# Kernel optimization log

Hardware: AMD Instinct MI355X
Metric: run time of the kernel (lower is better)

Reference implementation:

```python
import jax, jax.numpy as jnp
import numpy as np

HIDDEN = 768
INNER = 512
EPS = 1e-5


def setup_inputs() -> dict:
    key = jax.random.key(0)
    ks = jax.random.split(key, 6)
    B, S = 8, 4096
    x = jax.random.normal(ks[0], (B, S, HIDDEN), dtype=jnp.float32)
    W1 = jax.random.normal(ks[1], (INNER, HIDDEN), dtype=jnp.float32) * 0.02
    b1 = jnp.zeros((INNER,), dtype=jnp.float32)
    W2 = jax.random.normal(ks[2], (HIDDEN, INNER), dtype=jnp.float32) * 0.02
    b2 = jnp.zeros((HIDDEN,), dtype=jnp.float32)
    # output_proj: nn.Linear(hidden, hidden)
    bound = 1.0 / np.sqrt(HIDDEN)
    Wo = jax.random.uniform(ks[3], (HIDDEN, HIDDEN), minval=-bound, maxval=bound, dtype=jnp.float32)
    bo = jax.random.uniform(ks[4], (HIDDEN,), minval=-bound, maxval=bound, dtype=jnp.float32)
    # LayerNorm affine params
    gamma = jnp.ones((HIDDEN,), dtype=jnp.float32)
    beta = jnp.zeros((HIDDEN,), dtype=jnp.float32)
    return {"x": x, "W1": W1, "b1": b1, "W2": W2, "b2": b2,
            "Wo": Wo, "bo": bo, "gamma": gamma, "beta": beta}


def reference(x, W1, b1, W2, b2, Wo, bo, gamma, beta):
    # NOTE: the torch module's inner 'TTT update' loop never actually modifies
    # W1/b1/W2/b2 (loss computed, no step applied), so the math per token is
    # independent and fully vectorizable across (batch, seq).
    h = jax.nn.relu(jnp.einsum('bsd,id->bsi', x, W1) + b1)       # [B,S,INNER]
    pred = jnp.einsum('bsi,di->bsd', h, W2) + b2                 # [B,S,HIDDEN]
    out = jnp.einsum('bsd,ed->bse', pred, Wo) + bo               # output_proj
    # LayerNorm over last dim
    mu = jnp.mean(out, axis=-1, keepdims=True)
    var = jnp.mean(jnp.square(out - mu), axis=-1, keepdims=True)
    out = (out - mu) * jax.lax.rsqrt(var + EPS) * gamma + beta
    return out
```

## Files before the change

### kernel.cpp

```cpp
#include <hip/hip_runtime.h>
#include <hip/hip_bf16.h>


#define HIDDEN 768
#define INNER  512

typedef __bf16 bf16_t;
typedef bf16_t bf16x8 __attribute__((ext_vector_type(8)));
typedef bf16_t bf16x4 __attribute__((ext_vector_type(4)));
typedef float  f32x4  __attribute__((ext_vector_type(4)));

__device__ __forceinline__ void async16(const void* g, void* lds) {
  __builtin_amdgcn_global_load_lds(
      (const __attribute__((address_space(1))) unsigned int*)g,
      (__attribute__((address_space(3))) unsigned int*)lds, 16, 0, 0);
}

__global__ __launch_bounds__(256)
void prep(const float* __restrict__ x, const float* __restrict__ W1,
          const float* __restrict__ W2, const float* __restrict__ Wo,
          const float* __restrict__ b2, const float* __restrict__ bo,
          bf16_t* __restrict__ xb, bf16_t* __restrict__ W1b,
          bf16_t* __restrict__ W2t, bf16_t* __restrict__ Wob,
          float* __restrict__ beq, int xb_blocks) {
  __shared__ float T[64][65];
  const int b = blockIdx.x, t = threadIdx.x;

  const float4* src; bf16x4* dst; int base;
  if (b < xb_blocks)           { src = (const float4*)x;  dst = (bf16x4*)xb;  base = b * 4096; }
  else if (b < xb_blocks + 24) { src = (const float4*)W1; dst = (bf16x4*)W1b; base = (b - xb_blocks) * 4096; }
  else if (b < xb_blocks + 60) { src = (const float4*)Wo; dst = (bf16x4*)Wob; base = (b - xb_blocks - 24) * 4096; }
  else if (b < xb_blocks + 156) {
    const int tile = b - xb_blocks - 60;
    const int d0 = (tile >> 3) << 6;
    const int i0 = (tile & 7) << 6;
#pragma unroll
    for (int j = 0; j < 4; ++j) {
      const int idx = j * 256 + t;
      const int r = idx >> 4, c4 = idx & 15;
      float4 v = *(const float4*)(W2 + (size_t)(d0 + r) * INNER + i0 + c4 * 4);
      T[r][c4 * 4 + 0] = v.x; T[r][c4 * 4 + 1] = v.y;
      T[r][c4 * 4 + 2] = v.z; T[r][c4 * 4 + 3] = v.w;
    }
    __syncthreads();
    const int i = t & 63, h4 = t >> 6;
    bf16x8 o0, o1;
#pragma unroll
    for (int c = 0; c < 8; ++c) { o0[c] = (bf16_t)T[h4 * 16 + c][i]; o1[c] = (bf16_t)T[h4 * 16 + 8 + c][i]; }
    bf16_t* orow = W2t + (size_t)(i0 + i) * HIDDEN + d0 + h4 * 16;
    *(bf16x8*)orow = o0;
    *(bf16x8*)(orow + 8) = o1;
    return;
  } else {
    const int e = (b - xb_blocks - 156) * 4 + (t >> 6);
    const int l = t & 63;
    float s = 0.f;
#pragma unroll
    for (int j = 0; j < 12; ++j) s += Wo[(size_t)e * HIDDEN + j * 64 + l] * b2[j * 64 + l];
#pragma unroll
    for (int off = 1; off < 64; off <<= 1) s += __shfl_xor(s, off, 64);
    if (l == 0) beq[e] = s + bo[e];
    return;
  }
#pragma unroll
  for (int i = 0; i < 16; ++i) {
    float4 v = src[base + i * 256 + t];
    bf16x4 o;
    o[0] = (bf16_t)v.x; o[1] = (bf16_t)v.y; o[2] = (bf16_t)v.z; o[3] = (bf16_t)v.w;
    dst[base + i * 256 + t] = o;
  }
}

__global__ __launch_bounds__(256, 2)
void gemm_weq(const bf16_t* __restrict__ A, const bf16_t* __restrict__ Bt,
              bf16_t* __restrict__ Cout) {
  constexpr int N_ = INNER, K_ = HIDDEN, NT = N_ / 128, T = K_ / 64;
  __shared__ __align__(16) bf16_t As[2][128 * 64];
  __shared__ __align__(16) bf16_t Bs[2][128 * 64];

  const int nb = blockIdx.x;
  const int m0 = (nb / NT) * 128;
  const int n0 = (nb % NT) * 128;

  const int tid = threadIdx.x;
  const int w = tid >> 6, l = tid & 63;
  const int wr = w >> 1, wc = w & 1;
  const int fr = l & 15, fq = l >> 4;

#define STAGEW(dst, src, r0, k0)                                              \
  _Pragma("unroll") for (int i = 0; i < 4; ++i) {                             \
    const int G = i * 256 + tid, row = G >> 3, g = G & 7;                     \
    async16((src) + (size_t)((r0) + row) * K_ + (k0) + ((g ^ (row & 7)) << 3),\
            (char*)(dst) + (size_t)(i * 256 + w * 64) * 16);                  \
  }

  STAGEW(As[0], A, m0, 0); STAGEW(Bs[0], Bt, n0, 0);
  __syncthreads();

  f32x4 acc[4][4] = {};
#pragma unroll
  for (int t = 0; t < T; ++t) {
    const int cur = t & 1;
    if (t < T - 1) {
      STAGEW(As[cur ^ 1], A, m0, (t + 1) * 64);
      STAGEW(Bs[cur ^ 1], Bt, n0, (t + 1) * 64);
    }
#pragma unroll
    for (int kk = 0; kk < 2; ++kk) {
      bf16x8 ax[4], bx[4];
#pragma unroll
      for (int m = 0; m < 4; ++m) {
        const int row = wr * 64 + m * 16 + fr;
        const int slot = (kk * 4 + fq) ^ (row & 7);
        ax[m] = *(const bf16x8*)((const char*)As[cur] + row * 128 + slot * 16);
      }
#pragma unroll
      for (int n = 0; n < 4; ++n) {
        const int row = wc * 64 + n * 16 + fr;
        const int slot = (kk * 4 + fq) ^ (row & 7);
        bx[n] = *(const bf16x8*)((const char*)Bs[cur] + row * 128 + slot * 16);
      }
#pragma unroll
      for (int m = 0; m < 4; ++m)
#pragma unroll
        for (int n = 0; n < 4; ++n)
          acc[m][n] = __builtin_amdgcn_mfma_f32_16x16x32_bf16(ax[m], bx[n], acc[m][n], 0, 0, 0);
    }
    __syncthreads();
  }
#undef STAGEW

  const int orow0 = m0 + wr * 64 + fq * 4;
  const int ocol0 = n0 + wc * 64 + fr;
#pragma unroll
  for (int n = 0; n < 4; ++n)
#pragma unroll
    for (int m = 0; m < 4; ++m)
#pragma unroll
      for (int j = 0; j < 4; ++j)
        Cout[(size_t)(orow0 + m * 16 + j) * N_ + ocol0 + n * 16] = (bf16_t)acc[m][n][j];
}

template <int N_, int K_, int MODE>
__global__ __launch_bounds__(256, 2)
void gemm_bt(const bf16_t* __restrict__ A, const bf16_t* __restrict__ Bt,
             const float* __restrict__ bias, bf16_t* __restrict__ Cout) {
  constexpr int NT = N_ / 128;
  constexpr int T  = K_ / 64;
  __shared__ __align__(16) bf16_t As[2][128 * 64];
  __shared__ __align__(16) bf16_t Bs[2][128 * 64];

  const int per = gridDim.x >> 3;
  const int nb  = (blockIdx.x & 7) * per + (blockIdx.x >> 3);
  const int m0 = (nb / NT) * 128;
  const int n0 = (nb % NT) * 128;

  const int tid = threadIdx.x;
  const int w = tid >> 6, l = tid & 63;
  const int wr = w >> 1, wc = w & 1;
  const int fr = l & 15, fq = l >> 4;

#define STAGE(dst, src, r0, k0)                                               \
  _Pragma("unroll") for (int i = 0; i < 4; ++i) {                             \
    const int G = i * 256 + tid, row = G >> 3, g = G & 7;                     \
    async16((src) + (size_t)((r0) + row) * K_ + (k0) + ((g ^ (row & 7)) << 3),\
            (char*)(dst) + (size_t)(i * 256 + w * 64) * 16);                  \
  }

  STAGE(As[0], A, m0, 0); STAGE(Bs[0], Bt, n0, 0);

  f32x4 acc[4][4] = {};
#pragma unroll
  for (int t = 0; t < T; ++t) {
    const int cur = t & 1;
    if (t + 1 < T) {
      STAGE(As[cur ^ 1], A, m0, (t + 1) * 64);
      STAGE(Bs[cur ^ 1], Bt, n0, (t + 1) * 64);
      asm volatile("s_waitcnt vmcnt(8)" ::: "memory");
    } else {
      asm volatile("s_waitcnt vmcnt(0)" ::: "memory");
    }
    __builtin_amdgcn_s_barrier();
#pragma unroll
    for (int kk = 0; kk < 2; ++kk) {
      bf16x8 ax[4], bx[4];
#pragma unroll
      for (int m = 0; m < 4; ++m) {
        const int row = wr * 64 + m * 16 + fr;
        const int slot = (kk * 4 + fq) ^ (row & 7);
        ax[m] = *(const bf16x8*)((const char*)As[cur] + row * 128 + slot * 16);
      }
#pragma unroll
      for (int n = 0; n < 4; ++n) {
        const int row = wc * 64 + n * 16 + fr;
        const int slot = (kk * 4 + fq) ^ (row & 7);
        bx[n] = *(const bf16x8*)((const char*)Bs[cur] + row * 128 + slot * 16);
      }
#pragma unroll
      for (int m = 0; m < 4; ++m)
#pragma unroll
        for (int n = 0; n < 4; ++n)
          acc[m][n] = __builtin_amdgcn_mfma_f32_16x16x32_bf16(ax[m], bx[n], acc[m][n], 0, 0, 0);
    }
    __builtin_amdgcn_s_barrier();
  }
#undef STAGE

  const int orow0 = m0 + wr * 64 + fq * 4;
  const int ocol0 = n0 + wc * 64 + fr;
#pragma unroll
  for (int n = 0; n < 4; ++n) {
    const int col = ocol0 + n * 16;
    const float bv = bias[col];
#pragma unroll
    for (int m = 0; m < 4; ++m)
#pragma unroll
      for (int j = 0; j < 4; ++j) {
        float v = acc[m][n][j] + bv;
        if (MODE == 0) v = fmaxf(v, 0.f);
        Cout[(size_t)(orow0 + m * 16 + j) * N_ + col] = (bf16_t)v;
      }
  }
}

__global__ __launch_bounds__(256)
void ln_bf16(const bf16_t* __restrict__ raw, const float* __restrict__ gamma,
             const float* __restrict__ beta, float* __restrict__ out) {
  const int r = blockIdx.x * 4 + (threadIdx.x >> 6);
  const int l = threadIdx.x & 63;
  const bf16_t* rp = raw + (size_t)r * HIDDEN;
  float v[12];
  float s = 0.f, q = 0.f;
#pragma unroll
  for (int c = 0; c < 3; ++c) {
    bf16x4 b4 = *(const bf16x4*)(rp + c * 256 + l * 4);
#pragma unroll
    for (int j = 0; j < 4; ++j) {
      const float f = (float)b4[j];
      v[c * 4 + j] = f; s += f; q += f * f;
    }
  }
#pragma unroll
  for (int off = 1; off < 64; off <<= 1) {
    s += __shfl_xor(s, off, 64);
    q += __shfl_xor(q, off, 64);
  }
  const float mu  = s * (1.0f / HIDDEN);
  const float var = fmaxf(q * (1.0f / HIDDEN) - mu * mu, 0.f);
  const float inv = rsqrtf(var + 1e-5f);
  float* op = out + (size_t)r * HIDDEN;
#pragma unroll
  for (int c = 0; c < 3; ++c) {
    float4 g = ((const float4*)gamma)[c * 64 + l];
    float4 b = ((const float4*)beta)[c * 64 + l];
    float4 o;
    o.x = (v[c * 4 + 0] - mu) * inv * g.x + b.x;
    o.y = (v[c * 4 + 1] - mu) * inv * g.y + b.y;
    o.z = (v[c * 4 + 2] - mu) * inv * g.z + b.z;
    o.w = (v[c * 4 + 3] - mu) * inv * g.w + b.w;
    ((float4*)op)[c * 64 + l] = o;
  }
}

extern "C" void kernel_launch(void* const* d_in, const int* in_sizes, int n_in,
                              void* d_out, int out_size, void* d_ws, size_t ws_size,
                              hipStream_t stream) {
  const float* x     = (const float*)d_in[0];
  const float* W1    = (const float*)d_in[1];
  const float* b1    = (const float*)d_in[2];
  const float* W2    = (const float*)d_in[3];
  const float* b2    = (const float*)d_in[4];
  const float* Wo    = (const float*)d_in[5];
  const float* bo    = (const float*)d_in[6];
  const float* gamma = (const float*)d_in[7];
  const float* beta  = (const float*)d_in[8];

  const int M = in_sizes[0] / HIDDEN;

  char* ws = (char*)d_ws;
  bf16_t* xb   = (bf16_t*)ws;
  bf16_t* raw  = xb;
  bf16_t* h    = (bf16_t*)(ws + (size_t)M * HIDDEN * 2);
  bf16_t* W1b  = (bf16_t*)(ws + (size_t)M * HIDDEN * 2 + (size_t)M * INNER * 2);
  bf16_t* W2t  = W1b + INNER * HIDDEN;
  bf16_t* Wob  = W2t + INNER * HIDDEN;
  bf16_t* Weq  = Wob + HIDDEN * HIDDEN;
  float*  beq  = (float*)(Weq + HIDDEN * INNER);

  const int xb_blocks = (M * HIDDEN / 4) / 4096;

  prep<<<xb_blocks + 156 + 192, 256, 0, stream>>>(x, W1, W2, Wo, b2, bo,
                                                  xb, W1b, W2t, Wob, beq, xb_blocks);
  gemm_weq<<<(HIDDEN / 128) * (INNER / 128), 256, 0, stream>>>(Wob, W2t, Weq);
  gemm_bt<INNER, HIDDEN, 0><<<(M / 128) * (INNER / 128), 256, 0, stream>>>(xb, W1b, b1, h);
  gemm_bt<HIDDEN, INNER, 1><<<(M / 128) * (HIDDEN / 128), 256, 0, stream>>>(h, Weq, beq, raw);
  ln_bf16<<<M / 4, 256, 0, stream>>>(raw, gamma, beta, (float*)d_out);
}
```

Measured before the change: 133.0 us.

## Enlarge GEMM tiles to 256x256 with 512-thread blocks and raise MFMA priority

Replaces the 128x128, 256-thread GEMM kernel with a 256x256 tile kernel using 8 waves, each computing 128x64 of output. Larger tiles raise arithmetic intensity and cut redundant global and L2 reads of A and B. The LDS read order is restructured so B fragments are loaded once and A fragments are streamed per row block, and s_setprio is raised around the MFMA section. The cost is 128KB of LDS per block and more accumulator registers, which leaves one block per CU and fewer blocks overall (256 or 384 for M=32768).

```diff
diff --git a/kernel.cpp b/kernel.cpp
--- a/kernel.cpp
+++ b/kernel.cpp
@@ -142,78 +142,82 @@
 }
 
 template <int N_, int K_, int MODE>
-__global__ __launch_bounds__(256, 2)
-void gemm_bt(const bf16_t* __restrict__ A, const bf16_t* __restrict__ Bt,
+__global__ __launch_bounds__(512, 1)
+void gemm256(const bf16_t* __restrict__ A, const bf16_t* __restrict__ Bt,
              const float* __restrict__ bias, bf16_t* __restrict__ Cout) {
-  constexpr int NT = N_ / 128;
+  constexpr int NT = N_ / 256;
   constexpr int T  = K_ / 64;
-  __shared__ __align__(16) bf16_t As[2][128 * 64];
-  __shared__ __align__(16) bf16_t Bs[2][128 * 64];
+  __shared__ __align__(16) bf16_t As[2][256 * 64];
+  __shared__ __align__(16) bf16_t Bs[2][256 * 64];
 
   const int per = gridDim.x >> 3;
   const int nb  = (blockIdx.x & 7) * per + (blockIdx.x >> 3);
-  const int m0 = (nb / NT) * 128;
-  const int n0 = (nb % NT) * 128;
+  const int m0 = (nb / NT) * 256;
+  const int n0 = (nb % NT) * 256;
 
   const int tid = threadIdx.x;
   const int w = tid >> 6, l = tid & 63;
-  const int wr = w >> 1, wc = w & 1;
+  const int wm = w >> 2, wn = w & 3;
   const int fr = l & 15, fq = l >> 4;
 
-#define STAGE(dst, src, r0, k0)                                               \
+#define STG(dst, src, r0, k0)                                                 \
   _Pragma("unroll") for (int i = 0; i < 4; ++i) {                             \
-    const int G = i * 256 + tid, row = G >> 3, g = G & 7;                     \
+    const int G = i * 512 + tid, row = G >> 3, g = G & 7;                     \
     async16((src) + (size_t)((r0) + row) * K_ + (k0) + ((g ^ (row & 7)) << 3),\
-            (char*)(dst) + (size_t)(i * 256 + w * 64) * 16);                  \
-  }
-
-  STAGE(As[0], A, m0, 0); STAGE(Bs[0], Bt, n0, 0);
-
-  f32x4 acc[4][4] = {};
+            (char*)(dst) + (size_t)(i * 512 + w * 64) * 16);                  \
+  }
+
+  STG(As[0], A, m0, 0); STG(Bs[0], Bt, n0, 0);
+
+  f32x4 acc[8][4] = {};
 #pragma unroll
   for (int t = 0; t < T; ++t) {
     const int cur = t & 1;
     if (t + 1 < T) {
-      STAGE(As[cur ^ 1], A, m0, (t + 1) * 64);
-      STAGE(Bs[cur ^ 1], Bt, n0, (t + 1) * 64);
+      STG(As[cur ^ 1], A, m0, (t + 1) * 64);
+      STG(Bs[cur ^ 1], Bt, n0, (t + 1) * 64);
       asm volatile("s_waitcnt vmcnt(8)" ::: "memory");
     } else {
       asm volatile("s_waitcnt vmcnt(0)" ::: "memory");
     }
     __builtin_amdgcn_s_barrier();
-#pragma unroll
-    for (int kk = 0; kk < 2; ++kk) {
-      bf16x8 ax[4], bx[4];
-#pragma unroll
-      for (int m = 0; m < 4; ++m) {
-        const int row = wr * 64 + m * 16 + fr;
+
+    __builtin_amdgcn_s_setprio(1);
+    bf16x8 bx[4][2];
+#pragma unroll
+    for (int n = 0; n < 4; ++n)
+#pragma unroll
+      for (int kk = 0; kk < 2; ++kk) {
+        const int row = wn * 64 + n * 16 + fr;
         const int slot = (kk * 4 + fq) ^ (row & 7);
-        ax[m] = *(const bf16x8*)((const char*)As[cur] + row * 128 + slot * 16);
-      }
+        bx[n][kk] = *(const bf16x8*)((const char*)Bs[cur] + row * 128 + slot * 16);
+      }
+#pragma unroll
+    for (int m = 0; m < 8; ++m) {
+      const int row = wm * 128 + m * 16 + fr;
+      const int s0 = fq ^ (row & 7);
+      const int s1 = (4 + fq) ^ (row & 7);
+      bf16x8 ax0 = *(const bf16x8*)((const char*)As[cur] + row * 128 + s0 * 16);
+      bf16x8 ax1 = *(const bf16x8*)((const char*)As[cur] + row * 128 + s1 * 16);
 #pragma unroll
       for (int n = 0; n < 4; ++n) {
-        const int row = wc * 64 + n * 16 + fr;
-        const int slot = (kk * 4 + fq) ^ (row & 7);
-        bx[n] = *(const bf16x8*)((const char*)Bs[cur] + row * 128 + slot * 16);
-      }
-#pragma unroll
-      for (int m = 0; m < 4; ++m)
-#pragma unroll
-        for (int n = 0; n < 4; ++n)
-          acc[m][n] = __builtin_amdgcn_mfma_f32_16x16x32_bf16(ax[m], bx[n], acc[m][n], 0, 0, 0);
-    }
+        acc[m][n] = __builtin_amdgcn_mfma_f32_16x16x32_bf16(ax0, bx[n][0], acc[m][n], 0, 0, 0);
+        acc[m][n] = __builtin_amdgcn_mfma_f32_16x16x32_bf16(ax1, bx[n][1], acc[m][n], 0, 0, 0);
+      }
+    }
+    __builtin_amdgcn_s_setprio(0);
     __builtin_amdgcn_s_barrier();
   }
-#undef STAGE
-
-  const int orow0 = m0 + wr * 64 + fq * 4;
-  const int ocol0 = n0 + wc * 64 + fr;
+#undef STG
+
+  const int orow0 = m0 + wm * 128 + fq * 4;
+  const int ocol0 = n0 + wn * 64 + fr;
 #pragma unroll
   for (int n = 0; n < 4; ++n) {
     const int col = ocol0 + n * 16;
     const float bv = bias[col];
 #pragma unroll
-    for (int m = 0; m < 4; ++m)
+    for (int m = 0; m < 8; ++m)
 #pragma unroll
       for (int j = 0; j < 4; ++j) {
         float v = acc[m][n][j] + bv;
@@ -292,7 +296,7 @@
   prep<<<xb_blocks + 156 + 192, 256, 0, stream>>>(x, W1, W2, Wo, b2, bo,
                                                   xb, W1b, W2t, Wob, beq, xb_blocks);
   gemm_weq<<<(HIDDEN / 128) * (INNER / 128), 256, 0, stream>>>(Wob, W2t, Weq);
-  gemm_bt<INNER, HIDDEN, 0><<<(M / 128) * (INNER / 128), 256, 0, stream>>>(xb, W1b, b1, h);
-  gemm_bt<HIDDEN, INNER, 1><<<(M / 128) * (HIDDEN / 128), 256, 0, stream>>>(h, Weq, beq, raw);
+  gemm256<INNER, HIDDEN, 0><<<(M / 256) * (INNER / 256), 512, 0, stream>>>(xb, W1b, b1, h);
+  gemm256<HIDDEN, INNER, 1><<<(M / 256) * (HIDDEN / 256), 512, 0, stream>>>(h, Weq, beq, raw);
   ln_bf16<<<M / 4, 256, 0, stream>>>(raw, gamma, beta, (float*)d_out);
 }
```

Measured after the change: 138.9 us. 4.5% more time.

## Fold Weq weight-product GEMM into prep kernel, dropping separate launch

Applied to the files above, without the earlier changes.

The product Wo·W2 is now computed directly inside the prep kernel by 24 blocks. These blocks read the fp32 weights straight from global memory, converting and transposing them on the fly, instead of first writing bf16 copies and then running a separate LDS-pipelined GEMM kernel. This removes one kernel launch and the intermediate Wob/W2t buffers. The cost is that the new blocks do uncached, strided scalar loads of W2 with no LDS staging, and they may become a long tail inside prep. The elementwise conversion path also batches all 16 loads before converting them, to expose more memory parallelism.

```diff
diff --git a/kernel.cpp b/kernel.cpp
--- a/kernel.cpp
+++ b/kernel.cpp
@@ -21,38 +21,57 @@
           const float* __restrict__ W2, const float* __restrict__ Wo,
           const float* __restrict__ b2, const float* __restrict__ bo,
           bf16_t* __restrict__ xb, bf16_t* __restrict__ W1b,
-          bf16_t* __restrict__ W2t, bf16_t* __restrict__ Wob,
-          float* __restrict__ beq, int xb_blocks) {
-  __shared__ float T[64][65];
+          bf16_t* __restrict__ Weq, float* __restrict__ beq, int xb_blocks) {
   const int b = blockIdx.x, t = threadIdx.x;
 
-  const float4* src; bf16x4* dst; int base;
-  if (b < xb_blocks)           { src = (const float4*)x;  dst = (bf16x4*)xb;  base = b * 4096; }
-  else if (b < xb_blocks + 24) { src = (const float4*)W1; dst = (bf16x4*)W1b; base = (b - xb_blocks) * 4096; }
-  else if (b < xb_blocks + 60) { src = (const float4*)Wo; dst = (bf16x4*)Wob; base = (b - xb_blocks - 24) * 4096; }
-  else if (b < xb_blocks + 156) {
-    const int tile = b - xb_blocks - 60;
-    const int d0 = (tile >> 3) << 6;
-    const int i0 = (tile & 7) << 6;
-#pragma unroll
-    for (int j = 0; j < 4; ++j) {
-      const int idx = j * 256 + t;
-      const int r = idx >> 4, c4 = idx & 15;
-      float4 v = *(const float4*)(W2 + (size_t)(d0 + r) * INNER + i0 + c4 * 4);
-      T[r][c4 * 4 + 0] = v.x; T[r][c4 * 4 + 1] = v.y;
-      T[r][c4 * 4 + 2] = v.z; T[r][c4 * 4 + 3] = v.w;
-    }
-    __syncthreads();
-    const int i = t & 63, h4 = t >> 6;
-    bf16x8 o0, o1;
-#pragma unroll
-    for (int c = 0; c < 8; ++c) { o0[c] = (bf16_t)T[h4 * 16 + c][i]; o1[c] = (bf16_t)T[h4 * 16 + 8 + c][i]; }
-    bf16_t* orow = W2t + (size_t)(i0 + i) * HIDDEN + d0 + h4 * 16;
-    *(bf16x8*)orow = o0;
-    *(bf16x8*)(orow + 8) = o1;
+  if (b < 24) {
+    const int m0 = (b >> 2) * 128;
+    const int n0 = (b & 3) * 128;
+    const int w = t >> 6, l = t & 63;
+    const int wr = w >> 1, wc = w & 1;
+    const int fr = l & 15, fq = l >> 4;
+
+    f32x4 acc[4][4] = {};
+    for (int k0 = 0; k0 < HIDDEN; k0 += 32) {
+      bf16x8 ax[4], bx[4];
+#pragma unroll
+      for (int m = 0; m < 4; ++m) {
+        const float* ap = Wo + (size_t)(m0 + wr * 64 + m * 16 + fr) * HIDDEN + k0 + fq * 8;
+        f32x4 p0 = *(const f32x4*)ap;
+        f32x4 p1 = *(const f32x4*)(ap + 4);
+        bf16x8 a;
+#pragma unroll
+        for (int c = 0; c < 4; ++c) { a[c] = (bf16_t)p0[c]; a[4 + c] = (bf16_t)p1[c]; }
+        ax[m] = a;
+      }
+#pragma unroll
+      for (int n = 0; n < 4; ++n) {
+        const float* bp = W2 + (size_t)(k0 + fq * 8) * INNER + n0 + wc * 64 + n * 16 + fr;
+        bf16x8 v;
+#pragma unroll
+        for (int c = 0; c < 8; ++c) v[c] = (bf16_t)bp[(size_t)c * INNER];
+        bx[n] = v;
+      }
+#pragma unroll
+      for (int m = 0; m < 4; ++m)
+#pragma unroll
+        for (int n = 0; n < 4; ++n)
+          acc[m][n] = __builtin_amdgcn_mfma_f32_16x16x32_bf16(ax[m], bx[n], acc[m][n], 0, 0, 0);
+    }
+    const int orow0 = m0 + wr * 64 + fq * 4;
+    const int ocol0 = n0 + wc * 64 + fr;
+#pragma unroll
+    for (int n = 0; n < 4; ++n)
+#pragma unroll
+      for (int m = 0; m < 4; ++m)
+#pragma unroll
+        for (int j = 0; j < 4; ++j)
+          Weq[(size_t)(orow0 + m * 16 + j) * INNER + ocol0 + n * 16] = (bf16_t)acc[m][n][j];
     return;
-  } else {
-    const int e = (b - xb_blocks - 156) * 4 + (t >> 6);
+  }
+
+  if (b >= 48 + xb_blocks) {
+    const int e = (b - 48 - xb_blocks) * 4 + (t >> 6);
     const int l = t & 63;
     float s = 0.f;
 #pragma unroll
@@ -62,83 +81,21 @@
     if (l == 0) beq[e] = s + bo[e];
     return;
   }
+
+  const float4* src; bf16x4* dst; int base;
+  if (b < 48) { src = (const float4*)W1; dst = (bf16x4*)W1b; base = (b - 24) * 4096; }
+  else        { src = (const float4*)x;  dst = (bf16x4*)xb;  base = (b - 48) * 4096; }
+
+  f32x4 v[16];
+#pragma unroll
+  for (int i = 0; i < 16; ++i) v[i] = *(const f32x4*)&src[base + i * 256 + t];
 #pragma unroll
   for (int i = 0; i < 16; ++i) {
-    float4 v = src[base + i * 256 + t];
     bf16x4 o;
-    o[0] = (bf16_t)v.x; o[1] = (bf16_t)v.y; o[2] = (bf16_t)v.z; o[3] = (bf16_t)v.w;
+    o[0] = (bf16_t)v[i][0]; o[1] = (bf16_t)v[i][1];
+    o[2] = (bf16_t)v[i][2]; o[3] = (bf16_t)v[i][3];
     dst[base + i * 256 + t] = o;
   }
-}
-
-__global__ __launch_bounds__(256, 2)
-void gemm_weq(const bf16_t* __restrict__ A, const bf16_t* __restrict__ Bt,
-              bf16_t* __restrict__ Cout) {
-  constexpr int N_ = INNER, K_ = HIDDEN, NT = N_ / 128, T = K_ / 64;
-  __shared__ __align__(16) bf16_t As[2][128 * 64];
-  __shared__ __align__(16) bf16_t Bs[2][128 * 64];
-
-  const int nb = blockIdx.x;
-  const int m0 = (nb / NT) * 128;
-  const int n0 = (nb % NT) * 128;
-
-  const int tid = threadIdx.x;
-  const int w = tid >> 6, l = tid & 63;
-  const int wr = w >> 1, wc = w & 1;
-  const int fr = l & 15, fq = l >> 4;
-
-#define STAGEW(dst, src, r0, k0)                                              \
-  _Pragma("unroll") for (int i = 0; i < 4; ++i) {                             \
-    const int G = i * 256 + tid, row = G >> 3, g = G & 7;                     \
-    async16((src) + (size_t)((r0) + row) * K_ + (k0) + ((g ^ (row & 7)) << 3),\
-            (char*)(dst) + (size_t)(i * 256 + w * 64) * 16);                  \
-  }
-
-  STAGEW(As[0], A, m0, 0); STAGEW(Bs[0], Bt, n0, 0);
-  __syncthreads();
-
-  f32x4 acc[4][4] = {};
-#pragma unroll
-  for (int t = 0; t < T; ++t) {
-    const int cur = t & 1;
-    if (t < T - 1) {
-      STAGEW(As[cur ^ 1], A, m0, (t + 1) * 64);
-      STAGEW(Bs[cur ^ 1], Bt, n0, (t + 1) * 64);
-    }
-#pragma unroll
-    for (int kk = 0; kk < 2; ++kk) {
-      bf16x8 ax[4], bx[4];
-#pragma unroll
-      for (int m = 0; m < 4; ++m) {
-        const int row = wr * 64 + m * 16 + fr;
-        const int slot = (kk * 4 + fq) ^ (row & 7);
-        ax[m] = *(const bf16x8*)((const char*)As[cur] + row * 128 + slot * 16);
-      }
-#pragma unroll
-      for (int n = 0; n < 4; ++n) {
-        const int row = wc * 64 + n * 16 + fr;
-        const int slot = (kk * 4 + fq) ^ (row & 7);
-        bx[n] = *(const bf16x8*)((const char*)Bs[cur] + row * 128 + slot * 16);
-      }
-#pragma unroll
-      for (int m = 0; m < 4; ++m)
-#pragma unroll
-        for (int n = 0; n < 4; ++n)
-          acc[m][n] = __builtin_amdgcn_mfma_f32_16x16x32_bf16(ax[m], bx[n], acc[m][n], 0, 0, 0);
-    }
-    __syncthreads();
-  }
-#undef STAGEW
-
-  const int orow0 = m0 + wr * 64 + fq * 4;
-  const int ocol0 = n0 + wc * 64 + fr;
-#pragma unroll
-  for (int n = 0; n < 4; ++n)
-#pragma unroll
-    for (int m = 0; m < 4; ++m)
-#pragma unroll
-      for (int j = 0; j < 4; ++j)
-        Cout[(size_t)(orow0 + m * 16 + j) * N_ + ocol0 + n * 16] = (bf16_t)acc[m][n][j];
 }
 
 template <int N_, int K_, int MODE>
@@ -282,16 +239,13 @@
   bf16_t* raw  = xb;
   bf16_t* h    = (bf16_t*)(ws + (size_t)M * HIDDEN * 2);
   bf16_t* W1b  = (bf16_t*)(ws + (size_t)M * HIDDEN * 2 + (size_t)M * INNER * 2);
-  bf16_t* W2t  = W1b + INNER * HIDDEN;
-  bf16_t* Wob  = W2t + INNER * HIDDEN;
-  bf16_t* Weq  = Wob + HIDDEN * HIDDEN;
+  bf16_t* Weq  = W1b + INNER * HIDDEN;
   float*  beq  = (float*)(Weq + HIDDEN * INNER);
 
   const int xb_blocks = (M * HIDDEN / 4) / 4096;
 
-  prep<<<xb_blocks + 156 + 192, 256, 0, stream>>>(x, W1, W2, Wo, b2, bo,
-                                                  xb, W1b, W2t, Wob, beq, xb_blocks);
-  gemm_weq<<<(HIDDEN / 128) * (INNER / 128), 256, 0, stream>>>(Wob, W2t, Weq);
+  prep<<<48 + xb_blocks + 192, 256, 0, stream>>>(x, W1, W2, Wo, b2, bo,
+                                                 xb, W1b, Weq, beq, xb_blocks);
   gemm_bt<INNER, HIDDEN, 0><<<(M / 128) * (INNER / 128), 256, 0, stream>>>(xb, W1b, b1, h);
   gemm_bt<HIDDEN, INNER, 1><<<(M / 128) * (HIDDEN / 128), 256, 0, stream>>>(h, Weq, beq, raw);
   ln_bf16<<<M / 4, 256, 0, stream>>>(raw, gamma, beta, (float*)d_out);
```

New measurement: 135.2 us. About the same (+1.7%).
